# Kernel optimization log

Hardware: AMD Instinct MI355X
Metric: run time of the kernel (lower is better)

Reference implementation:

```python
import jax, jax.numpy as jnp
import numpy as np

B, C, H, W = 2, 512, 64, 64
S = 2            # scale_factor
HEADS = 8
GROUPS = 32      # assumed GroupNorm groups for group_norm(in_channels)
DK = C // HEADS
SCALE = 1.0 / DK ** 2   # faithful to source: 1/d_k**2
RES = H // S
R = RES * 2 - 1


def setup_inputs() -> dict:
    key = jax.random.key(0)
    ks = jax.random.split(key, 8)
    f = lambda k, shp, s=0.02: jax.random.normal(k, shp, jnp.float32) * s
    return {
        "x": jax.random.normal(ks[0], (B, C, H, W), jnp.float32),
        "q_w": f(ks[1], (C, C, 1, 1)),
        "q_b": jnp.zeros((C,), jnp.float32),
        "kv_w": f(ks[2], (2 * C, C, 1, 1)),
        "kv_b": jnp.zeros((2 * C,), jnp.float32),
        "off1_w": f(ks[3], (C, C, S, S)),
        "off1_b": jnp.zeros((C,), jnp.float32),
        "gn_w": jnp.ones((C,), jnp.float32),
        "gn_b": jnp.zeros((C,), jnp.float32),
        "off2_w": f(ks[4], (2, C, 1, 1)),
        "rpe_table": f(ks[5], (HEADS, R, R), 0.01),
        "proj_w": f(ks[6], (C, C, 1, 1)),
        "proj_b": jnp.zeros((C,), jnp.float32),
    }


def _conv(x, w, b=None, stride=1):
    y = jax.lax.conv_general_dilated(x, w, (stride, stride), 'VALID',
                                     dimension_numbers=('NCHW', 'OIHW', 'NCHW'))
    return y if b is None else y + b[None, :, None, None]


def _group_norm(x, w, b, eps=1e-5):
    n, c, h, wd = x.shape
    xg = x.reshape(n, GROUPS, -1)
    mu = xg.mean(-1, keepdims=True)
    var = xg.var(-1, keepdims=True)
    xg = (xg - mu) * jax.lax.rsqrt(var + eps)
    return xg.reshape(n, c, h, wd) * w[None, :, None, None] + b[None, :, None, None]


def _grid_sample(img, grid):
    # bilinear, align_corners=True; img [B,C,H,W], grid [B,...,2] in (x,y) order
    Bn, Cn, Hn, Wn = img.shape
    gshape = grid.shape[1:-1]
    g = grid.reshape(Bn, -1, 2)
    x = (g[..., 0] + 1.0) * 0.5 * (Wn - 1)
    y = (g[..., 1] + 1.0) * 0.5 * (Hn - 1)
    x0 = jnp.floor(x); y0 = jnp.floor(y)
    wx = (x - x0)[:, None, :]; wy = (y - y0)[:, None, :]
    x0i = jnp.clip(x0.astype(jnp.int32), 0, Wn - 1)
    x1i = jnp.clip(x0i + 1, 0, Wn - 1)
    y0i = jnp.clip(y0.astype(jnp.int32), 0, Hn - 1)
    y1i = jnp.clip(y0i + 1, 0, Hn - 1)
    imf = img.reshape(Bn, Cn, Hn * Wn)
    gat = lambda yi, xi: jnp.take_along_axis(imf, (yi * Wn + xi)[:, None, :], axis=2)
    out = (gat(y0i, x0i) * (1 - wx) * (1 - wy) + gat(y0i, x1i) * wx * (1 - wy)
           + gat(y1i, x0i) * (1 - wx) * wy + gat(y1i, x1i) * wx * wy)
    return out.reshape(Bn, Cn, *gshape)


def _forward(x, q_w, q_b, kv_w, kv_b, off1_w, off1_b, gn_w, gn_b, off2_w,
             rpe_table, proj_w, proj_b):
    l = H * W
    q = _conv(x, q_w, q_b)                                   # [B,C,H,W]
    t = _conv(q, off1_w, off1_b, stride=S)                   # [B,C,h,w]
    t = jax.nn.gelu(_group_norm(t, gn_w, gn_b), approximate=False)
    offset = _conv(t, off2_w).transpose(0, 2, 3, 1)          # [B,h,w,2] (y,x)
    h, w = offset.shape[1], offset.shape[2]
    n = h * w
    # reference points (linspace 0.5..h-0.5, normalized by h-1)
    ry = (jnp.linspace(0.5, h - 0.5, h) / (h - 1.0)) * 2.0 - 1.0
    rx = (jnp.linspace(0.5, w - 0.5, w) / (w - 1.0)) * 2.0 - 1.0
    ref = jnp.stack(jnp.meshgrid(ry, rx, indexing='ij'), -1)  # [h,w,2]
    pos = jnp.clip(offset + ref[None], -1.0, 1.0)             # [B,h,w,2]
    sampled = _grid_sample(x, pos[..., ::-1])                 # [B,C,h,w] (context=x)
    kv = _conv(sampled.reshape(B, C, 1, n), kv_w, kv_b)       # [B,2C,1,n]
    k, v = kv[:, :C], kv[:, C:]
    qf = q.reshape(B * HEADS, DK, l)
    kf = k.reshape(B * HEADS, DK, n)
    vf = v.reshape(B * HEADS, DK, n)
    attn = jnp.einsum('bcm,bcn->bmn', qf, kf) * SCALE         # [B*H, l, n]
    # query grid (arange, normalized by dim-1)
    gy = jnp.arange(H, dtype=jnp.float32) / (H - 1.0) * 2.0 - 1.0
    gx = jnp.arange(W, dtype=jnp.float32) / (W - 1.0) * 2.0 - 1.0
    qg = jnp.stack(jnp.meshgrid(gy, gx, indexing='ij'), -1).reshape(l, 2)
    disp = (qg[None, :, None, :] - pos.reshape(B, 1, n, 2)) * 0.5  # [B,l,n,2]
    rpe = jnp.broadcast_to(rpe_table[None], (B, HEADS, R, R))
    bias = _grid_sample(rpe, disp[..., ::-1])                  # [B,HEADS,l,n]
    attn = jax.nn.softmax(attn + bias.reshape(B * HEADS, l, n), axis=-1)
    out = jnp.einsum('bmn,bcn->bcm', attn, vf).reshape(B, C, H, W)
    return _conv(out, proj_w, proj_b)


def reference(x, q_w, q_b, kv_w, kv_b, off1_w, off1_b, gn_w, gn_b, off2_w,
              rpe_table, proj_w, proj_b):
    return _forward(x, q_w, q_b, kv_w, kv_b, off1_w, off1_b, gn_w, gn_b,
                    off2_w, rpe_table, proj_w, proj_b)
```

## Files before the change

kernel.cpp:

```cpp
#include <hip/hip_runtime.h>
#include <hip/hip_bf16.h>
#include <math.h>

typedef float floatx4 __attribute__((ext_vector_type(4)));
typedef short shortx8 __attribute__((ext_vector_type(8)));
typedef unsigned short ush;

#define NB    2
#define NC    512
#define NL    4096
#define NN    1024
#define NH    8
#define NDK   64
#define NR    63
#define SCALE_ (1.0f/4096.0f)

#define OFF_Q      0u
#define OFF_T      4194304u
#define OFF_GS     5242880u
#define OFF_POS    5243904u
#define OFF_SMP    5248000u
#define OFF_KV     5772288u
#define OFF_PART   6820864u
#define OFF_AO     6820864u

__device__ __forceinline__ ush f2bf(float f) {
    unsigned u = __float_as_uint(f);
    u += 0x7fffu + ((u >> 16) & 1u);
    return (ush)(u >> 16);
}
__device__ __forceinline__ float bf2f(ush h) {
    return __uint_as_float(((unsigned)h) << 16);
}

template<int NP, int BSRC, int OUTMODE>
__global__ __launch_bounds__(256) void gemm_mfma_k(
    const float* __restrict__ A, const void* __restrict__ Bv,
    const float* __restrict__ bias, void* __restrict__ Yv,
    int M, int K, int P, int KS)
{
    __shared__ ush a_hi[128 * 72];
    __shared__ ush b_hi[64 * 72];
    __shared__ ush a_lo[NP == 3 ? 128 * 72 : 64];
    __shared__ ush b_lo[NP == 3 ? 64 * 72 : 64];

    int tid = threadIdx.x;
    int wv = tid >> 6, lane = tid & 63, quad = lane >> 4, l15 = lane & 15;
    int bz = blockIdx.z;
    int b = bz / KS, ks = bz - b * KS;
    int m0 = blockIdx.y * 128, p0 = blockIdx.x * 64;
    int Ksl = K / KS, kbeg = ks * Ksl;

    floatx4 acc[2][4];
    #pragma unroll
    for (int mt = 0; mt < 2; ++mt)
        #pragma unroll
        for (int pt = 0; pt < 4; ++pt) acc[mt][pt] = (floatx4)0.f;

    for (int kc = 0; kc < Ksl; kc += 64) {
        int kg0 = kbeg + kc;
        #pragma unroll
        for (int r = 0; r < 8; ++r) {
            int idx = r * 256 + tid;
            int m = idx >> 4, k4 = (idx & 15) << 2;
            float4 av = *(const float4*)(A + (size_t)(m0 + m) * K + kg0 + k4);
            int o = m * 72 + k4;
            ush h0 = f2bf(av.x), h1 = f2bf(av.y), h2 = f2bf(av.z), h3 = f2bf(av.w);
            a_hi[o] = h0; a_hi[o + 1] = h1; a_hi[o + 2] = h2; a_hi[o + 3] = h3;
            if (NP == 3) {
                a_lo[o]     = f2bf(av.x - bf2f(h0));
                a_lo[o + 1] = f2bf(av.y - bf2f(h1));
                a_lo[o + 2] = f2bf(av.z - bf2f(h2));
                a_lo[o + 3] = f2bf(av.w - bf2f(h3));
            }
        }
        #pragma unroll
        for (int r = 0; r < 8; ++r) {
            int idx = r * 256 + tid;
            int k = idx >> 5, p2 = (idx & 31) << 1;
            float v0, v1;
            if (BSRC == 0) {
                const float* Bp = (const float*)Bv + (size_t)b * K * P;
                float2 t2 = *(const float2*)(Bp + (size_t)(kg0 + k) * P + p0 + p2);
                v0 = t2.x; v1 = t2.y;
            } else if (BSRC == 1) {
                const float* Bp = (const float*)Bv + (size_t)b * NC * NL;
                int kk = kg0 + k;
                int c = kk >> 2, kh = (kk >> 1) & 1, kw = kk & 1;
                int p = p0 + p2;
                int oh = p >> 5, ow = p & 31;
                const float* base = Bp + (size_t)c * NL + (2 * oh + kh) * 64 + kw;
                v0 = base[2 * ow];
                v1 = base[2 * ow + 2];
            } else {
                const ush* Bp = (const ush*)Bv + (size_t)b * K * P;
                unsigned u = *(const unsigned*)(Bp + (size_t)(kg0 + k) * P + p0 + p2);
                v0 = bf2f((ush)(u & 0xffffu));
                v1 = bf2f((ush)(u >> 16));
            }
            ush h0 = f2bf(v0), h1 = f2bf(v1);
            b_hi[p2 * 72 + k] = h0;
            b_hi[(p2 + 1) * 72 + k] = h1;
            if (NP == 3) {
                b_lo[p2 * 72 + k]       = f2bf(v0 - bf2f(h0));
                b_lo[(p2 + 1) * 72 + k] = f2bf(v1 - bf2f(h1));
            }
        }
        __syncthreads();

        shortx8 ah[2][2], al[2][2];
        #pragma unroll
        for (int mt = 0; mt < 2; ++mt)
            #pragma unroll
            for (int kk = 0; kk < 2; ++kk) {
                int o = (wv * 32 + mt * 16 + l15) * 72 + kk * 32 + quad * 8;
                ah[mt][kk] = *(const shortx8*)&a_hi[o];
                if (NP == 3) al[mt][kk] = *(const shortx8*)&a_lo[o];
            }
        #pragma unroll
        for (int pt = 0; pt < 4; ++pt) {
            #pragma unroll
            for (int kk = 0; kk < 2; ++kk) {
                int o = (pt * 16 + l15) * 72 + kk * 32 + quad * 8;
                shortx8 bh = *(const shortx8*)&b_hi[o];
                acc[0][pt] = __builtin_amdgcn_mfma_f32_16x16x32_bf16(ah[0][kk], bh, acc[0][pt], 0, 0, 0);
                acc[1][pt] = __builtin_amdgcn_mfma_f32_16x16x32_bf16(ah[1][kk], bh, acc[1][pt], 0, 0, 0);
                if (NP == 3) {
                    shortx8 bl = *(const shortx8*)&b_lo[o];
                    acc[0][pt] = __builtin_amdgcn_mfma_f32_16x16x32_bf16(ah[0][kk], bl, acc[0][pt], 0, 0, 0);
                    acc[1][pt] = __builtin_amdgcn_mfma_f32_16x16x32_bf16(ah[1][kk], bl, acc[1][pt], 0, 0, 0);
                    acc[0][pt] = __builtin_amdgcn_mfma_f32_16x16x32_bf16(al[0][kk], bh, acc[0][pt], 0, 0, 0);
                    acc[1][pt] = __builtin_amdgcn_mfma_f32_16x16x32_bf16(al[1][kk], bh, acc[1][pt], 0, 0, 0);
                }
            }
        }
        __syncthreads();
    }

    #pragma unroll
    for (int mt = 0; mt < 2; ++mt) {
        #pragma unroll
        for (int reg = 0; reg < 4; ++reg) {
            int m = m0 + wv * 32 + mt * 16 + quad * 4 + reg;
            float bb = (OUTMODE == 2) ? 0.f : bias[m];
            #pragma unroll
            for (int pt = 0; pt < 4; ++pt) {
                int p = p0 + pt * 16 + l15;
                float val = acc[mt][pt][reg] + bb;
                if (OUTMODE == 0)
                    ((float*)Yv)[(size_t)b * M * P + (size_t)m * P + p] = val;
                else if (OUTMODE == 1)
                    ((ush*)Yv)[(size_t)b * M * P + (size_t)m * P + p] = f2bf(val);
                else
                    ((float*)Yv)[(size_t)(ks * NB + b) * M * P + (size_t)m * P + p] = val;
            }
        }
    }
}

__global__ __launch_bounds__(256) void reduce_off1_k(const float* __restrict__ part,
                                                     const float* __restrict__ bias,
                                                     float* __restrict__ t)
{
    int i = blockIdx.x * 256 + threadIdx.x;
    float v = part[i] + part[i + 1048576] + part[i + 2097152] + part[i + 3145728];
    t[i] = v + bias[(i >> 10) & 511];
}

__global__ __launch_bounds__(256) void gn_stats_k(const float* __restrict__ T, float* __restrict__ gs)
{
    int bg = blockIdx.x;
    const float* base = T + (size_t)bg * 16384;
    float s = 0.f, ss = 0.f;
    for (int i = threadIdx.x; i < 16384; i += 256) { float v = base[i]; s += v; ss += v * v; }
    #pragma unroll
    for (int off = 32; off >= 1; off >>= 1) { s += __shfl_xor(s, off); ss += __shfl_xor(ss, off); }
    __shared__ float red[8];
    int wv = threadIdx.x >> 6;
    if ((threadIdx.x & 63) == 0) { red[wv * 2] = s; red[wv * 2 + 1] = ss; }
    __syncthreads();
    if (threadIdx.x == 0) {
        float S = red[0] + red[2] + red[4] + red[6];
        float SS = red[1] + red[3] + red[5] + red[7];
        float mu = S / 16384.f;
        float var = SS / 16384.f - mu * mu;
        gs[bg * 2] = mu;
        gs[bg * 2 + 1] = rsqrtf(var + 1e-5f);
    }
}

__global__ __launch_bounds__(256) void gn_gelu_k(float* __restrict__ T, const float* __restrict__ gs,
                                                 const float* __restrict__ gw, const float* __restrict__ gb)
{
    int idx = blockIdx.x * 256 + threadIdx.x;
    int bg = idx >> 14;
    int c = (idx >> 10) & 511;
    float mu = gs[bg * 2], rs = gs[bg * 2 + 1];
    float v = (T[idx] - mu) * rs * gw[c] + gb[c];
    T[idx] = v * 0.5f * (1.f + erff(v * 0.70710678118654752f));
}

__global__ __launch_bounds__(256) void offset_pos_k(const float* __restrict__ T,
                                                    const float* __restrict__ w2,
                                                    float* __restrict__ pos)
{
    int idx = blockIdx.x * 256 + threadIdx.x;
    int b = idx >> 10, op = idx & 1023;
    const float* Tb = T + (size_t)b * NC * NN;
    float o0 = 0.f, o1 = 0.f;
    for (int ci = 0; ci < NC; ++ci) {
        float tv = Tb[(size_t)ci * NN + op];
        o0 += w2[ci] * tv;
        o1 += w2[NC + ci] * tv;
    }
    int oh = op >> 5, ow = op & 31;
    float ry = (0.5f + oh) / 31.0f * 2.f - 1.f;
    float rx = (0.5f + ow) / 31.0f * 2.f - 1.f;
    pos[idx * 2]     = fminf(fmaxf(o0 + ry, -1.f), 1.f);
    pos[idx * 2 + 1] = fminf(fmaxf(o1 + rx, -1.f), 1.f);
}

__global__ __launch_bounds__(256) void sample_k(const float* __restrict__ x,
                                                const float* __restrict__ pos,
                                                ush* __restrict__ smp)
{
    int idx = blockIdx.x * 256 + threadIdx.x;
    int j = idx & 1023, c = (idx >> 10) & 511, b = idx >> 19;
    float py = pos[(b * 1024 + j) * 2];
    float px = pos[(b * 1024 + j) * 2 + 1];
    float fx = (px + 1.f) * 0.5f * 63.f;
    float fy = (py + 1.f) * 0.5f * 63.f;
    float flx = floorf(fx), fly = floorf(fy);
    float wx = fx - flx, wy = fy - fly;
    int x0 = min(max((int)flx, 0), 63), y0 = min(max((int)fly, 0), 63);
    int x1 = min(x0 + 1, 63),           y1 = min(y0 + 1, 63);
    const float* xb = x + ((size_t)(b * NC + c)) * NL;
    float v00 = xb[y0 * 64 + x0];
    float v01 = xb[y0 * 64 + x1];
    float v10 = xb[y1 * 64 + x0];
    float v11 = xb[y1 * 64 + x1];
    float v = v00 * (1 - wx) * (1 - wy) + v01 * wx * (1 - wy)
            + v10 * (1 - wx) * wy       + v11 * wx * wy;
    smp[idx] = f2bf(v);
}

__global__ __launch_bounds__(256) void attn_k(
    const float* __restrict__ q, const ush* __restrict__ kv,
    const float* __restrict__ pos, const float* __restrict__ rpe,
    ush* __restrict__ out)
{
    __shared__ __align__(16) char smem[63760];
    ush*   qa    = (ush*)smem;
    ush*   kt    = (ush*)(smem + 18432);
    ush*   vs    = (ush*)(smem + 27648);
    ush*   pa    = (ush*)(smem + 36864);
    ush*   rpe_s = (ush*)(smem + 55296);
    float* posj  = (float*)(smem + 63248);
    float* obuf  = (float*)smem;

    int bh = blockIdx.y;
    int b = bh >> 3, h = bh & 7;
    int m0 = blockIdx.x * 128;
    const float* qh = q  + ((size_t)(b * NC + h * NDK)) * NL;
    const ush* kh = kv + ((size_t)(b * 2 * NC + h * NDK)) * NN;
    const ush* vh = kv + ((size_t)(b * 2 * NC + NC + h * NDK)) * NN;
    ush* oh_ = out + ((size_t)(b * NC + h * NDK)) * NL;
    const float* posb = pos + (size_t)b * 2048;

    int tid = threadIdx.x;
    int wv = tid >> 6, lane = tid & 63, quad = lane >> 4, l15 = lane & 15;

    for (int i = tid; i < NR * NR; i += 256) rpe_s[i] = f2bf(rpe[(size_t)h * NR * NR + i]);
    for (int i = tid; i < 4096; i += 256) {
        int d = i >> 6, mp = (i & 63) << 1;
        float2 t2 = *(const float2*)(qh + (size_t)d * NL + m0 + mp);
        qa[mp * 72 + d]       = f2bf(t2.x);
        qa[(mp + 1) * 72 + d] = f2bf(t2.y);
    }

    float qgy[2][4], qgx[2][4];
    #pragma unroll
    for (int mt = 0; mt < 2; ++mt)
        #pragma unroll
        for (int reg = 0; reg < 4; ++reg) {
            int mg = m0 + wv * 32 + mt * 16 + quad * 4 + reg;
            qgy[mt][reg] = (float)(mg >> 6) * (2.f / 63.f) - 1.f;
            qgx[mt][reg] = (float)(mg & 63) * (2.f / 63.f) - 1.f;
        }

    float m_run[2][4], l_run[2][4], alpha[2][4];
    floatx4 o_acc[2][4];
    #pragma unroll
    for (int mt = 0; mt < 2; ++mt)
        #pragma unroll
        for (int r = 0; r < 4; ++r) { m_run[mt][r] = -1e30f; l_run[mt][r] = 0.f; }
    #pragma unroll
    for (int mt = 0; mt < 2; ++mt)
        #pragma unroll
        for (int dt = 0; dt < 4; ++dt) o_acc[mt][dt] = (floatx4)0.f;

    __syncthreads();

    for (int jc = 0; jc < 16; ++jc) {
        int j0 = jc * 64;
        for (int i = tid; i < 2048; i += 256) {
            int d = i >> 5, jp = (i & 31) << 1;
            unsigned k2 = *(const unsigned*)(kh + (size_t)d * NN + j0 + jp);
            kt[jp * 72 + d]       = (ush)(k2 & 0xffffu);
            kt[(jp + 1) * 72 + d] = (ush)(k2 >> 16);
            unsigned v2 = *(const unsigned*)(vh + (size_t)d * NN + j0 + jp);
            vs[d * 72 + jp]     = (ush)(v2 & 0xffffu);
            vs[d * 72 + jp + 1] = (ush)(v2 >> 16);
        }
        if (tid < 128) posj[tid] = posb[j0 * 2 + tid];
        __syncthreads();

        shortx8 qf[2][2];
        #pragma unroll
        for (int mt = 0; mt < 2; ++mt)
            #pragma unroll
            for (int ks = 0; ks < 2; ++ks)
                qf[mt][ks] = *(const shortx8*)(qa + (wv * 32 + mt * 16 + l15) * 72 + ks * 32 + quad * 8);
        floatx4 sacc[2][4];
        #pragma unroll
        for (int mt = 0; mt < 2; ++mt)
            #pragma unroll
            for (int jt = 0; jt < 4; ++jt) sacc[mt][jt] = (floatx4)0.f;
        #pragma unroll
        for (int jt = 0; jt < 4; ++jt) {
            #pragma unroll
            for (int ks = 0; ks < 2; ++ks) {
                shortx8 kf = *(const shortx8*)(kt + (jt * 16 + l15) * 72 + ks * 32 + quad * 8);
                sacc[0][jt] = __builtin_amdgcn_mfma_f32_16x16x32_bf16(qf[0][ks], kf, sacc[0][jt], 0, 0, 0);
                sacc[1][jt] = __builtin_amdgcn_mfma_f32_16x16x32_bf16(qf[1][ks], kf, sacc[1][jt], 0, 0, 0);
            }
        }

        #pragma unroll
        for (int jt = 0; jt < 4; ++jt) {
            float2 pp = ((const float2*)posj)[jt * 16 + l15];
            #pragma unroll
            for (int mt = 0; mt < 2; ++mt) {
                #pragma unroll
                for (int reg = 0; reg < 4; ++reg) {
                    float gy = (qgy[mt][reg] - pp.x) * 15.5f + 31.f;
                    float gx = (qgx[mt][reg] - pp.y) * 15.5f + 31.f;
                    float fy = floorf(gy), fx = floorf(gx);
                    float wy = gy - fy, wx = gx - fx;
                    int y0c = min(max((int)fy, 0), 62), x0c = min(max((int)fx, 0), 62);
                    int y1c = min(y0c + 1, 62),         x1c = min(x0c + 1, 62);
                    int ry0 = y0c * 63, ry1 = y1c * 63;
                    float r00 = bf2f(rpe_s[ry0 + x0c]);
                    float r01 = bf2f(rpe_s[ry0 + x1c]);
                    float r10 = bf2f(rpe_s[ry1 + x0c]);
                    float r11 = bf2f(rpe_s[ry1 + x1c]);
                    float ba = r00 + wx * (r01 - r00);
                    float bb = r10 + wx * (r11 - r10);
                    sacc[mt][jt][reg] = sacc[mt][jt][reg] * SCALE_ + (ba + wy * (bb - ba));
                }
            }
        }
        #pragma unroll
        for (int mt = 0; mt < 2; ++mt) {
            #pragma unroll
            for (int reg = 0; reg < 4; ++reg) {
                float mx = fmaxf(fmaxf(sacc[mt][0][reg], sacc[mt][1][reg]),
                                 fmaxf(sacc[mt][2][reg], sacc[mt][3][reg]));
                #pragma unroll
                for (int off = 8; off >= 1; off >>= 1) mx = fmaxf(mx, __shfl_xor(mx, off));
                float nm = fmaxf(m_run[mt][reg], mx);
                float a_ = __expf(m_run[mt][reg] - nm);
                float ps = 0.f;
                #pragma unroll
                for (int jt = 0; jt < 4; ++jt) {
                    float p = __expf(sacc[mt][jt][reg] - nm);
                    sacc[mt][jt][reg] = p;
                    ps += p;
                }
                #pragma unroll
                for (int off = 8; off >= 1; off >>= 1) ps += __shfl_xor(ps, off);
                l_run[mt][reg] = l_run[mt][reg] * a_ + ps;
                m_run[mt][reg] = nm;
                alpha[mt][reg] = a_;
            }
        }
        #pragma unroll
        for (int mt = 0; mt < 2; ++mt)
            #pragma unroll
            for (int jt = 0; jt < 4; ++jt)
                #pragma unroll
                for (int reg = 0; reg < 4; ++reg)
                    pa[(wv * 32 + mt * 16 + quad * 4 + reg) * 72 + jt * 16 + l15] =
                        f2bf(sacc[mt][jt][reg]);
        __syncthreads();

        #pragma unroll
        for (int mt = 0; mt < 2; ++mt)
            #pragma unroll
            for (int dt = 0; dt < 4; ++dt)
                #pragma unroll
                for (int reg = 0; reg < 4; ++reg)
                    o_acc[mt][dt][reg] *= alpha[mt][reg];
        shortx8 pf[2][2];
        #pragma unroll
        for (int mt = 0; mt < 2; ++mt)
            #pragma unroll
            for (int ks = 0; ks < 2; ++ks)
                pf[mt][ks] = *(const shortx8*)(pa + (wv * 32 + mt * 16 + l15) * 72 + ks * 32 + quad * 8);
        #pragma unroll
        for (int dt = 0; dt < 4; ++dt) {
            #pragma unroll
            for (int ks = 0; ks < 2; ++ks) {
                shortx8 vf = *(const shortx8*)(vs + (dt * 16 + l15) * 72 + ks * 32 + quad * 8);
                o_acc[0][dt] = __builtin_amdgcn_mfma_f32_16x16x32_bf16(pf[0][ks], vf, o_acc[0][dt], 0, 0, 0);
                o_acc[1][dt] = __builtin_amdgcn_mfma_f32_16x16x32_bf16(pf[1][ks], vf, o_acc[1][dt], 0, 0, 0);
            }
        }
        __syncthreads();
    }

    #pragma unroll
    for (int mt = 0; mt < 2; ++mt) {
        float inv[4];
        #pragma unroll
        for (int reg = 0; reg < 4; ++reg) inv[reg] = 1.f / l_run[mt][reg];
        #pragma unroll
        for (int dt = 0; dt < 4; ++dt)
            #pragma unroll
            for (int reg = 0; reg < 4; ++reg)
                obuf[(dt * 16 + l15) * 132 + wv * 32 + mt * 16 + quad * 4 + reg] =
                    o_acc[mt][dt][reg] * inv[reg];
    }
    __syncthreads();
    for (int i = tid; i < 8192; i += 256) {
        int d = i >> 7, m = i & 127;
        oh_[(size_t)d * NL + m0 + m] = f2bf(obuf[d * 132 + m]);
    }
}

extern "C" void kernel_launch(void* const* d_in, const int* in_sizes, int n_in,
                              void* d_out, int out_size, void* d_ws, size_t ws_size,
                              hipStream_t stream) {
    const float* x      = (const float*)d_in[0];
    const float* q_w    = (const float*)d_in[1];
    const float* q_b    = (const float*)d_in[2];
    const float* kv_w   = (const float*)d_in[3];
    const float* kv_b   = (const float*)d_in[4];
    const float* off1_w = (const float*)d_in[5];
    const float* off1_b = (const float*)d_in[6];
    const float* gn_w   = (const float*)d_in[7];
    const float* gn_b   = (const float*)d_in[8];
    const float* off2_w = (const float*)d_in[9];
    const float* rpe    = (const float*)d_in[10];
    const float* proj_w = (const float*)d_in[11];
    const float* proj_b = (const float*)d_in[12];

    float* ws   = (float*)d_ws;
    float* q    = ws + OFF_Q;
    float* t    = ws + OFF_T;
    float* gs   = ws + OFF_GS;
    float* pos  = ws + OFF_POS;
    ush*   smp  = (ush*)(ws + OFF_SMP);
    ush*   kvb  = (ush*)(ws + OFF_KV);
    float* part = ws + OFF_PART;
    ush*   ao   = (ush*)(ws + OFF_AO);
    float* out  = (float*)d_out;

    gemm_mfma_k<3, 0, 0><<<dim3(64, 4, 2), 256, 0, stream>>>(q_w, x, q_b, q, 512, 512, 4096, 1);
    gemm_mfma_k<3, 1, 2><<<dim3(16, 4, 8), 256, 0, stream>>>(off1_w, q, nullptr, part, 512, 2048, 1024, 4);
    reduce_off1_k<<<4096, 256, 0, stream>>>(part, off1_b, t);
    gn_stats_k<<<64, 256, 0, stream>>>(t, gs);
    gn_gelu_k<<<4096, 256, 0, stream>>>(t, gs, gn_w, gn_b);
    offset_pos_k<<<8, 256, 0, stream>>>(t, off2_w, pos);
    sample_k<<<4096, 256, 0, stream>>>(x, pos, smp);
    gemm_mfma_k<1, 2, 1><<<dim3(16, 8, 2), 256, 0, stream>>>(kv_w, smp, kv_b, kvb, 1024, 512, 1024, 1);
    attn_k<<<dim3(32, 16), 256, 0, stream>>>(q, kvb, pos, rpe, ao);
    gemm_mfma_k<1, 2, 0><<<dim3(64, 4, 2), 256, 0, stream>>>(proj_w, ao, proj_b, out, 512, 512, 4096, 1);
}
```

Baseline: 394.3 us.

## Restructure attention with pre-transposed Q/K/V, packed RPE table and max-free softmax

The Q-projection and KV-projection GEMM epilogues now also write bf16 Q (pre-scaled by log2e/d_k²), K and V in layouts the attention kernel reads directly from global memory. This removes the per-block LDS transposes and most of the barriers. Attention uses 64-row tiles and a precomputed 4-tap packed bf16 RPE table, so each bilinear lookup is one LDS read. It drops the running-max online softmax in favour of plain exp2, with the row sum computed by an MFMA against a ones vector. offset_pos is split across channel groups with an LDS reduction for more parallelism. The cost is overflow risk if logits grow large, plus strided transposed stores in the GEMM epilogues.

Result: faster. 368.6 us (-6.5%).

```diff
diff --git a/kernel.cpp b/kernel.cpp
--- a/kernel.cpp
+++ b/kernel.cpp
@@ -13,16 +13,20 @@
 #define NH    8
 #define NDK   64
 #define NR    63
-#define SCALE_ (1.0f/4096.0f)
+#define LOG2E 1.44269504f
+#define QT_SCALE (1.44269504f/4096.0f)
 
 #define OFF_Q      0u
-#define OFF_T      4194304u
-#define OFF_GS     5242880u
-#define OFF_POS    5243904u
-#define OFF_SMP    5248000u
-#define OFF_KV     5772288u
-#define OFF_PART   6820864u
-#define OFF_AO     6820864u
+#define OFF_AO     0u
+#define OFF_SMP    2097152u
+#define OFF_QT     4194304u
+#define OFF_T      6291456u
+#define OFF_GS     7340032u
+#define OFF_POS    7340160u
+#define OFF_KT     7344256u
+#define OFF_VV     7868544u
+#define OFF_PART   8392832u
+#define OFF_TAB4   8392832u
 
 __device__ __forceinline__ ush f2bf(float f) {
     unsigned u = __float_as_uint(f);
@@ -36,7 +40,7 @@
 template<int NP, int BSRC, int OUTMODE>
 __global__ __launch_bounds__(256) void gemm_mfma_k(
     const float* __restrict__ A, const void* __restrict__ Bv,
-    const float* __restrict__ bias, void* __restrict__ Yv,
+    const float* __restrict__ bias, void* __restrict__ Yv, void* __restrict__ Y2,
     int M, int K, int P, int KS)
 {
     __shared__ ush a_hi[128 * 72];
@@ -147,12 +151,23 @@
             for (int pt = 0; pt < 4; ++pt) {
                 int p = p0 + pt * 16 + l15;
                 float val = acc[mt][pt][reg] + bb;
-                if (OUTMODE == 0)
+                if (OUTMODE == 0) {
                     ((float*)Yv)[(size_t)b * M * P + (size_t)m * P + p] = val;
-                else if (OUTMODE == 1)
-                    ((ush*)Yv)[(size_t)b * M * P + (size_t)m * P + p] = f2bf(val);
-                else
+                } else if (OUTMODE == 2) {
                     ((float*)Yv)[(size_t)(ks * NB + b) * M * P + (size_t)m * P + p] = val;
+                } else if (OUTMODE == 3) {
+                    ((float*)Yv)[(size_t)b * M * P + (size_t)m * P + p] = val;
+                    int h = m >> 6, d = m & 63;
+                    ((ush*)Y2)[(((size_t)(b * 8 + h) * 4096) + p) * 64 + d] = f2bf(val * QT_SCALE);
+                } else {
+                    if (m < 512) {
+                        int h = m >> 6, d = m & 63;
+                        ((ush*)Yv)[(((size_t)(b * 8 + h) * 1024) + p) * 64 + d] = f2bf(val);
+                    } else {
+                        int c = m - 512;
+                        ((ush*)Y2)[((size_t)(b * 512) + c) * 1024 + p] = f2bf(val);
+                    }
+                }
             }
         }
     }
@@ -204,20 +219,33 @@
                                                     const float* __restrict__ w2,
                                                     float* __restrict__ pos)
 {
-    int idx = blockIdx.x * 256 + threadIdx.x;
-    int b = idx >> 10, op = idx & 1023;
-    const float* Tb = T + (size_t)b * NC * NN;
+    int b = blockIdx.x >> 5;
+    int og = threadIdx.x & 31;
+    int cg = threadIdx.x >> 5;
+    int op = ((blockIdx.x & 31) << 5) + og;
+    const float* Tb = T + (size_t)b * NC * NN + (size_t)cg * 64 * NN + op;
     float o0 = 0.f, o1 = 0.f;
-    for (int ci = 0; ci < NC; ++ci) {
-        float tv = Tb[(size_t)ci * NN + op];
-        o0 += w2[ci] * tv;
-        o1 += w2[NC + ci] * tv;
-    }
-    int oh = op >> 5, ow = op & 31;
-    float ry = (0.5f + oh) / 31.0f * 2.f - 1.f;
-    float rx = (0.5f + ow) / 31.0f * 2.f - 1.f;
-    pos[idx * 2]     = fminf(fmaxf(o0 + ry, -1.f), 1.f);
-    pos[idx * 2 + 1] = fminf(fmaxf(o1 + rx, -1.f), 1.f);
+    #pragma unroll 4
+    for (int c = 0; c < 64; ++c) {
+        float tv = Tb[(size_t)c * NN];
+        o0 += w2[cg * 64 + c] * tv;
+        o1 += w2[512 + cg * 64 + c] * tv;
+    }
+    __shared__ float rs[2][8][32];
+    rs[0][cg][og] = o0;
+    rs[1][cg][og] = o1;
+    __syncthreads();
+    if (threadIdx.x < 64) {
+        int coord = threadIdx.x >> 5, og2 = threadIdx.x & 31;
+        float s = 0.f;
+        #pragma unroll
+        for (int k = 0; k < 8; ++k) s += rs[coord][k][og2];
+        int opf = ((blockIdx.x & 31) << 5) + og2;
+        int oh = opf >> 5, ow = opf & 31;
+        float ref = (coord == 0) ? ((0.5f + oh) / 31.f * 2.f - 1.f)
+                                 : ((0.5f + ow) / 31.f * 2.f - 1.f);
+        pos[((size_t)b * 1024 + opf) * 2 + coord] = fminf(fmaxf(s + ref, -1.f), 1.f);
+    }
 }
 
 __global__ __launch_bounds__(256) void sample_k(const float* __restrict__ x,
@@ -244,197 +272,132 @@
     smp[idx] = f2bf(v);
 }
 
+__global__ __launch_bounds__(256) void tab4_k(const float* __restrict__ rpe,
+                                              uint2* __restrict__ tab4)
+{
+    int i = blockIdx.x * 256 + threadIdx.x;
+    int h = i >> 12, y = (i >> 6) & 63, x = i & 63;
+    const float* R = rpe + (size_t)h * 3969;
+    float v00 = (y < 63 && x < 63)         ? R[y * 63 + x] * LOG2E : 0.f;
+    float v01 = (y < 63 && x + 1 < 63)     ? R[y * 63 + x + 1] * LOG2E : 0.f;
+    float v10 = (y + 1 < 63 && x < 63)     ? R[(y + 1) * 63 + x] * LOG2E : 0.f;
+    float v11 = (y + 1 < 63 && x + 1 < 63) ? R[(y + 1) * 63 + x + 1] * LOG2E : 0.f;
+    uint2 o;
+    o.x = (unsigned)f2bf(v00) | ((unsigned)f2bf(v01) << 16);
+    o.y = (unsigned)f2bf(v10) | ((unsigned)f2bf(v11) << 16);
+    tab4[i] = o;
+}
+
 __global__ __launch_bounds__(256) void attn_k(
-    const float* __restrict__ q, const ush* __restrict__ kv,
-    const float* __restrict__ pos, const float* __restrict__ rpe,
-    ush* __restrict__ out)
-{
-    __shared__ __align__(16) char smem[63760];
-    ush*   qa    = (ush*)smem;
-    ush*   kt    = (ush*)(smem + 18432);
-    ush*   vs    = (ush*)(smem + 27648);
-    ush*   pa    = (ush*)(smem + 36864);
-    ush*   rpe_s = (ush*)(smem + 55296);
-    float* posj  = (float*)(smem + 63248);
-    float* obuf  = (float*)smem;
+    const ush* __restrict__ qT, const ush* __restrict__ kT,
+    const ush* __restrict__ vv, const float* __restrict__ pos,
+    const uint2* __restrict__ tab4, ush* __restrict__ ao)
+{
+    __shared__ __align__(16) char smem[50176];
+    ush*   pa     = (ush*)smem;
+    uint2* tab_s  = (uint2*)(smem + 9216);
+    float* posj15 = (float*)(smem + 41984);
+    float* obuf   = (float*)smem;
 
     int bh = blockIdx.y;
     int b = bh >> 3, h = bh & 7;
-    int m0 = blockIdx.x * 128;
-    const float* qh = q  + ((size_t)(b * NC + h * NDK)) * NL;
-    const ush* kh = kv + ((size_t)(b * 2 * NC + h * NDK)) * NN;
-    const ush* vh = kv + ((size_t)(b * 2 * NC + NC + h * NDK)) * NN;
-    ush* oh_ = out + ((size_t)(b * NC + h * NDK)) * NL;
-    const float* posb = pos + (size_t)b * 2048;
-
+    int m0 = blockIdx.x * 64;
     int tid = threadIdx.x;
     int wv = tid >> 6, lane = tid & 63, quad = lane >> 4, l15 = lane & 15;
 
-    for (int i = tid; i < NR * NR; i += 256) rpe_s[i] = f2bf(rpe[(size_t)h * NR * NR + i]);
-    for (int i = tid; i < 4096; i += 256) {
-        int d = i >> 6, mp = (i & 63) << 1;
-        float2 t2 = *(const float2*)(qh + (size_t)d * NL + m0 + mp);
-        qa[mp * 72 + d]       = f2bf(t2.x);
-        qa[(mp + 1) * 72 + d] = f2bf(t2.y);
-    }
-
-    float qgy[2][4], qgx[2][4];
-    #pragma unroll
-    for (int mt = 0; mt < 2; ++mt)
-        #pragma unroll
-        for (int reg = 0; reg < 4; ++reg) {
-            int mg = m0 + wv * 32 + mt * 16 + quad * 4 + reg;
-            qgy[mt][reg] = (float)(mg >> 6) * (2.f / 63.f) - 1.f;
-            qgx[mt][reg] = (float)(mg & 63) * (2.f / 63.f) - 1.f;
-        }
-
-    float m_run[2][4], l_run[2][4], alpha[2][4];
-    floatx4 o_acc[2][4];
-    #pragma unroll
-    for (int mt = 0; mt < 2; ++mt)
-        #pragma unroll
-        for (int r = 0; r < 4; ++r) { m_run[mt][r] = -1e30f; l_run[mt][r] = 0.f; }
-    #pragma unroll
-    for (int mt = 0; mt < 2; ++mt)
-        #pragma unroll
-        for (int dt = 0; dt < 4; ++dt) o_acc[mt][dt] = (floatx4)0.f;
+    const ush* qbase = qT + ((size_t)bh * 4096 + m0 + wv * 16 + l15) * 64 + quad * 8;
+    shortx8 qf0 = *(const shortx8*)(qbase);
+    shortx8 qf1 = *(const shortx8*)(qbase + 32);
+
+    const uint2* tg = tab4 + (size_t)h * 4096;
+    for (int i = tid; i < 4096; i += 256) tab_s[i] = tg[i];
+    const float* pb = pos + (size_t)b * 2048;
+    for (int i = tid; i < 2048; i += 256) posj15[i] = pb[i] * 15.5f;
+
+    float qy15[4], qx15[4];
+    #pragma unroll
+    for (int reg = 0; reg < 4; ++reg) {
+        int mg = m0 + wv * 16 + quad * 4 + reg;
+        qy15[reg] = (float)(mg >> 6) * (31.f / 63.f) + 15.5f;
+        qx15[reg] = (float)(mg & 63) * (31.f / 63.f) + 15.5f;
+    }
+
+    floatx4 o_acc[4], o_sum;
+    #pragma unroll
+    for (int dt = 0; dt < 4; ++dt) o_acc[dt] = (floatx4)0.f;
+    o_sum = (floatx4)0.f;
+    shortx8 vone = {16256, 16256, 16256, 16256, 16256, 16256, 16256, 16256};
 
     __syncthreads();
+
+    const ush* kbase = kT + (size_t)bh * 1024 * 64;
+    const ush* vbase = vv + (size_t)(b * 512 + h * 64) * 1024;
 
     for (int jc = 0; jc < 16; ++jc) {
         int j0 = jc * 64;
-        for (int i = tid; i < 2048; i += 256) {
-            int d = i >> 5, jp = (i & 31) << 1;
-            unsigned k2 = *(const unsigned*)(kh + (size_t)d * NN + j0 + jp);
-            kt[jp * 72 + d]       = (ush)(k2 & 0xffffu);
-            kt[(jp + 1) * 72 + d] = (ush)(k2 >> 16);
-            unsigned v2 = *(const unsigned*)(vh + (size_t)d * NN + j0 + jp);
-            vs[d * 72 + jp]     = (ush)(v2 & 0xffffu);
-            vs[d * 72 + jp + 1] = (ush)(v2 >> 16);
-        }
-        if (tid < 128) posj[tid] = posb[j0 * 2 + tid];
-        __syncthreads();
-
-        shortx8 qf[2][2];
-        #pragma unroll
-        for (int mt = 0; mt < 2; ++mt)
-            #pragma unroll
-            for (int ks = 0; ks < 2; ++ks)
-                qf[mt][ks] = *(const shortx8*)(qa + (wv * 32 + mt * 16 + l15) * 72 + ks * 32 + quad * 8);
-        floatx4 sacc[2][4];
-        #pragma unroll
-        for (int mt = 0; mt < 2; ++mt)
-            #pragma unroll
-            for (int jt = 0; jt < 4; ++jt) sacc[mt][jt] = (floatx4)0.f;
+        floatx4 sacc[4];
+        #pragma unroll
+        for (int jt = 0; jt < 4; ++jt) sacc[jt] = (floatx4)0.f;
         #pragma unroll
         for (int jt = 0; jt < 4; ++jt) {
-            #pragma unroll
-            for (int ks = 0; ks < 2; ++ks) {
-                shortx8 kf = *(const shortx8*)(kt + (jt * 16 + l15) * 72 + ks * 32 + quad * 8);
-                sacc[0][jt] = __builtin_amdgcn_mfma_f32_16x16x32_bf16(qf[0][ks], kf, sacc[0][jt], 0, 0, 0);
-                sacc[1][jt] = __builtin_amdgcn_mfma_f32_16x16x32_bf16(qf[1][ks], kf, sacc[1][jt], 0, 0, 0);
-            }
-        }
-
+            const ush* kp = kbase + (size_t)(j0 + jt * 16 + l15) * 64 + quad * 8;
+            shortx8 kf0 = *(const shortx8*)kp;
+            shortx8 kf1 = *(const shortx8*)(kp + 32);
+            sacc[jt] = __builtin_amdgcn_mfma_f32_16x16x32_bf16(qf0, kf0, sacc[jt], 0, 0, 0);
+            sacc[jt] = __builtin_amdgcn_mfma_f32_16x16x32_bf16(qf1, kf1, sacc[jt], 0, 0, 0);
+        }
         #pragma unroll
         for (int jt = 0; jt < 4; ++jt) {
-            float2 pp = ((const float2*)posj)[jt * 16 + l15];
-            #pragma unroll
-            for (int mt = 0; mt < 2; ++mt) {
-                #pragma unroll
-                for (int reg = 0; reg < 4; ++reg) {
-                    float gy = (qgy[mt][reg] - pp.x) * 15.5f + 31.f;
-                    float gx = (qgx[mt][reg] - pp.y) * 15.5f + 31.f;
-                    float fy = floorf(gy), fx = floorf(gx);
-                    float wy = gy - fy, wx = gx - fx;
-                    int y0c = min(max((int)fy, 0), 62), x0c = min(max((int)fx, 0), 62);
-                    int y1c = min(y0c + 1, 62),         x1c = min(x0c + 1, 62);
-                    int ry0 = y0c * 63, ry1 = y1c * 63;
-                    float r00 = bf2f(rpe_s[ry0 + x0c]);
-                    float r01 = bf2f(rpe_s[ry0 + x1c]);
-                    float r10 = bf2f(rpe_s[ry1 + x0c]);
-                    float r11 = bf2f(rpe_s[ry1 + x1c]);
-                    float ba = r00 + wx * (r01 - r00);
-                    float bb = r10 + wx * (r11 - r10);
-                    sacc[mt][jt][reg] = sacc[mt][jt][reg] * SCALE_ + (ba + wy * (bb - ba));
-                }
-            }
-        }
-        #pragma unroll
-        for (int mt = 0; mt < 2; ++mt) {
+            int j = j0 + jt * 16 + l15;
+            float2 pp = *(const float2*)&posj15[j * 2];
             #pragma unroll
             for (int reg = 0; reg < 4; ++reg) {
-                float mx = fmaxf(fmaxf(sacc[mt][0][reg], sacc[mt][1][reg]),
-                                 fmaxf(sacc[mt][2][reg], sacc[mt][3][reg]));
-                #pragma unroll
-                for (int off = 8; off >= 1; off >>= 1) mx = fmaxf(mx, __shfl_xor(mx, off));
-                float nm = fmaxf(m_run[mt][reg], mx);
-                float a_ = __expf(m_run[mt][reg] - nm);
-                float ps = 0.f;
-                #pragma unroll
-                for (int jt = 0; jt < 4; ++jt) {
-                    float p = __expf(sacc[mt][jt][reg] - nm);
-                    sacc[mt][jt][reg] = p;
-                    ps += p;
-                }
-                #pragma unroll
-                for (int off = 8; off >= 1; off >>= 1) ps += __shfl_xor(ps, off);
-                l_run[mt][reg] = l_run[mt][reg] * a_ + ps;
-                m_run[mt][reg] = nm;
-                alpha[mt][reg] = a_;
-            }
-        }
-        #pragma unroll
-        for (int mt = 0; mt < 2; ++mt)
-            #pragma unroll
-            for (int jt = 0; jt < 4; ++jt)
-                #pragma unroll
-                for (int reg = 0; reg < 4; ++reg)
-                    pa[(wv * 32 + mt * 16 + quad * 4 + reg) * 72 + jt * 16 + l15] =
-                        f2bf(sacc[mt][jt][reg]);
-        __syncthreads();
-
-        #pragma unroll
-        for (int mt = 0; mt < 2; ++mt)
-            #pragma unroll
-            for (int dt = 0; dt < 4; ++dt)
-                #pragma unroll
-                for (int reg = 0; reg < 4; ++reg)
-                    o_acc[mt][dt][reg] *= alpha[mt][reg];
-        shortx8 pf[2][2];
-        #pragma unroll
-        for (int mt = 0; mt < 2; ++mt)
-            #pragma unroll
-            for (int ks = 0; ks < 2; ++ks)
-                pf[mt][ks] = *(const shortx8*)(pa + (wv * 32 + mt * 16 + l15) * 72 + ks * 32 + quad * 8);
+                float gy = qy15[reg] - pp.x;
+                float gx = qx15[reg] - pp.y;
+                float fy = floorf(gy), fx = floorf(gx);
+                float wy = gy - fy, wx = gx - fx;
+                int y0 = min(max((int)fy, 0), 62);
+                int x0 = min(max((int)fx, 0), 62);
+                uint2 tw = tab_s[(y0 << 6) + x0];
+                float r00 = __uint_as_float(tw.x << 16);
+                float r01 = __uint_as_float(tw.x & 0xffff0000u);
+                float r10 = __uint_as_float(tw.y << 16);
+                float r11 = __uint_as_float(tw.y & 0xffff0000u);
+                float bx0 = r00 + wx * (r01 - r00);
+                float bx1 = r10 + wx * (r11 - r10);
+                float p = exp2f(sacc[jt][reg] + (bx0 + wy * (bx1 - bx0)));
+                pa[(wv * 16 + quad * 4 + reg) * 72 + jt * 16 + l15] = f2bf(p);
+            }
+        }
+        const ush* pbase = pa + (wv * 16 + l15) * 72 + quad * 8;
+        shortx8 pf0 = *(const shortx8*)pbase;
+        shortx8 pf1 = *(const shortx8*)(pbase + 32);
+        o_sum = __builtin_amdgcn_mfma_f32_16x16x32_bf16(pf0, vone, o_sum, 0, 0, 0);
+        o_sum = __builtin_amdgcn_mfma_f32_16x16x32_bf16(pf1, vone, o_sum, 0, 0, 0);
         #pragma unroll
         for (int dt = 0; dt < 4; ++dt) {
-            #pragma unroll
-            for (int ks = 0; ks < 2; ++ks) {
-                shortx8 vf = *(const shortx8*)(vs + (dt * 16 + l15) * 72 + ks * 32 + quad * 8);
-                o_acc[0][dt] = __builtin_amdgcn_mfma_f32_16x16x32_bf16(pf[0][ks], vf, o_acc[0][dt], 0, 0, 0);
-                o_acc[1][dt] = __builtin_amdgcn_mfma_f32_16x16x32_bf16(pf[1][ks], vf, o_acc[1][dt], 0, 0, 0);
-            }
-        }
-        __syncthreads();
-    }
-
-    #pragma unroll
-    for (int mt = 0; mt < 2; ++mt) {
-        float inv[4];
-        #pragma unroll
-        for (int reg = 0; reg < 4; ++reg) inv[reg] = 1.f / l_run[mt][reg];
-        #pragma unroll
-        for (int dt = 0; dt < 4; ++dt)
-            #pragma unroll
-            for (int reg = 0; reg < 4; ++reg)
-                obuf[(dt * 16 + l15) * 132 + wv * 32 + mt * 16 + quad * 4 + reg] =
-                    o_acc[mt][dt][reg] * inv[reg];
-    }
+            const ush* vp = vbase + (size_t)(dt * 16 + l15) * 1024 + j0 + quad * 8;
+            shortx8 vf0 = *(const shortx8*)vp;
+            shortx8 vf1 = *(const shortx8*)(vp + 32);
+            o_acc[dt] = __builtin_amdgcn_mfma_f32_16x16x32_bf16(pf0, vf0, o_acc[dt], 0, 0, 0);
+            o_acc[dt] = __builtin_amdgcn_mfma_f32_16x16x32_bf16(pf1, vf1, o_acc[dt], 0, 0, 0);
+        }
+    }
+
     __syncthreads();
-    for (int i = tid; i < 8192; i += 256) {
-        int d = i >> 7, m = i & 127;
-        oh_[(size_t)d * NL + m0 + m] = f2bf(obuf[d * 132 + m]);
+    float inv[4];
+    #pragma unroll
+    for (int reg = 0; reg < 4; ++reg) inv[reg] = 1.f / o_sum[reg];
+    #pragma unroll
+    for (int dt = 0; dt < 4; ++dt)
+        #pragma unroll
+        for (int reg = 0; reg < 4; ++reg)
+            obuf[(dt * 16 + l15) * 68 + wv * 16 + quad * 4 + reg] = o_acc[dt][reg] * inv[reg];
+    __syncthreads();
+    ush* aobase = ao + ((size_t)(b * 512 + h * 64)) * 4096 + m0;
+    for (int i = tid; i < 4096; i += 256) {
+        int d = i >> 6, m = i & 63;
+        aobase[(size_t)d * 4096 + m] = f2bf(obuf[d * 68 + m]);
     }
 }
 
@@ -457,23 +420,27 @@
 
     float* ws   = (float*)d_ws;
     float* q    = ws + OFF_Q;
+    ush*   ao   = (ush*)(ws + OFF_AO);
+    ush*   smp  = (ush*)(ws + OFF_SMP);
+    ush*   qT   = (ush*)(ws + OFF_QT);
     float* t    = ws + OFF_T;
     float* gs   = ws + OFF_GS;
     float* pos  = ws + OFF_POS;
-    ush*   smp  = (ush*)(ws + OFF_SMP);
-    ush*   kvb  = (ush*)(ws + OFF_KV);
+    ush*   kT   = (ush*)(ws + OFF_KT);
+    ush*   vv   = (ush*)(ws + OFF_VV);
     float* part = ws + OFF_PART;
-    ush*   ao   = (ush*)(ws + OFF_AO);
+    uint2* tab4 = (uint2*)(ws + OFF_TAB4);
     float* out  = (float*)d_out;
 
-    gemm_mfma_k<3, 0, 0><<<dim3(64, 4, 2), 256, 0, stream>>>(q_w, x, q_b, q, 512, 512, 4096, 1);
-    gemm_mfma_k<3, 1, 2><<<dim3(16, 4, 8), 256, 0, stream>>>(off1_w, q, nullptr, part, 512, 2048, 1024, 4);
+    gemm_mfma_k<3, 0, 3><<<dim3(64, 4, 2), 256, 0, stream>>>(q_w, x, q_b, q, qT, 512, 512, 4096, 1);
+    gemm_mfma_k<3, 1, 2><<<dim3(16, 4, 8), 256, 0, stream>>>(off1_w, q, nullptr, part, nullptr, 512, 2048, 1024, 4);
     reduce_off1_k<<<4096, 256, 0, stream>>>(part, off1_b, t);
     gn_stats_k<<<64, 256, 0, stream>>>(t, gs);
     gn_gelu_k<<<4096, 256, 0, stream>>>(t, gs, gn_w, gn_b);
-    offset_pos_k<<<8, 256, 0, stream>>>(t, off2_w, pos);
+    offset_pos_k<<<64, 256, 0, stream>>>(t, off2_w, pos);
+    tab4_k<<<128, 256, 0, stream>>>(rpe, tab4);
     sample_k<<<4096, 256, 0, stream>>>(x, pos, smp);
-    gemm_mfma_k<1, 2, 1><<<dim3(16, 8, 2), 256, 0, stream>>>(kv_w, smp, kv_b, kvb, 1024, 512, 1024, 1);
-    attn_k<<<dim3(32, 16), 256, 0, stream>>>(q, kvb, pos, rpe, ao);
-    gemm_mfma_k<1, 2, 0><<<dim3(64, 4, 2), 256, 0, stream>>>(proj_w, ao, proj_b, out, 512, 512, 4096, 1);
-}
+    gemm_mfma_k<1, 2, 4><<<dim3(16, 8, 2), 256, 0, stream>>>(kv_w, smp, kv_b, kT, vv, 1024, 512, 1024, 1);
+    attn_k<<<dim3(64, 16), 256, 0, stream>>>(qT, kT, vv, pos, tab4, ao);
+    gemm_mfma_k<1, 2, 0><<<dim3(64, 4, 2), 256, 0, stream>>>(proj_w, ao, proj_b, out, nullptr, 512, 512, 4096, 1);
+}
```
